# Optimization experiments

Measured on AMD Instinct MI355X. Metric: run time of the kernel, lower is better.

The kernel has to match this reference:

```python
import jax, jax.numpy as jnp
import numpy as np

T_, B_, DIM, NB, D, H_, W_ = 4, 4, 256, 16, 16, 32, 32
VTH_L1_LOW = VTH_L1_HIGH = 0.5
EPS = 1e-5

# ---- surrogate-gradient spike (ATan surrogate, alpha=2.0, spikingjelly default) ----
@jax.custom_vjp
def spike(x):
    return (x >= 0).astype(x.dtype)

def _spk_fwd(x):
    return spike(x), x

def _spk_bwd(x, g):
    a = 2.0
    return (g * (a / 2.0) / (1.0 + (jnp.pi / 2.0 * a * x) ** 2),)

spike.defvjp(_spk_fwd, _spk_bwd)

def lif(x, tau=2.0, vth=1.0):
    # MultiStepLIFNode: v += (x - v)/tau; fire at vth; hard reset (detach_reset)
    def step(v, xt):
        v = v + (xt - v) / tau
        s = spike(v - vth)
        v = v * (1.0 - jax.lax.stop_gradient(s))
        return v, s
    _, s = jax.lax.scan(step, jnp.zeros_like(x[0]), x)
    return s

def haar_mat(n):
    m = np.zeros((n, n), np.float32)
    s = 1.0 / np.sqrt(2.0)
    for i in range(n // 2):
        m[i, 2 * i] = s; m[i, 2 * i + 1] = s          # low-pass rows
        m[n // 2 + i, 2 * i] = s; m[n // 2 + i, 2 * i + 1] = -s  # high-pass rows
    return jnp.asarray(m)

def bn(x, g, b):  # training-mode BatchNorm2d over (N,C,H,W)
    mu = jnp.mean(x, axis=(0, 2, 3), keepdims=True)
    var = jnp.var(x, axis=(0, 2, 3), keepdims=True)
    return g.reshape(1, -1, 1, 1) * (x - mu) * jax.lax.rsqrt(var + EPS) + b.reshape(1, -1, 1, 1)

def conv(x, w, b):
    y = jax.lax.conv_general_dilated(x, w, (1, 1), 'SAME',
                                     dimension_numbers=('NCHW', 'OIHW', 'NCHW'))
    return y + b.reshape(1, -1, 1, 1)

def band_gate(c, vth, tau):
    # coefficient spiking threshold then channel-energy sparsity gate
    c = c * spike(jnp.abs(c) - vth)
    E = jnp.mean(c * c, axis=(-2, -1), keepdims=True)  # per (T,B,C) energy
    return c * (E > tau).astype(c.dtype)

def _forward(x, haar_weight, conv1_w, conv1_b, conv2_w, conv2_b,
             bn_fwd_g, bn_fwd_b, bn_mul_g, bn_mul_b, bn_inv_g, bn_inv_b,
             bn_c1_g, bn_c1_b, bn_c2_g, bn_c2_b):
    T, B, C, H, W = x.shape
    HmW, HmH = haar_mat(W), haar_mat(H)
    Hh, Wh, TB = H // 2, W // 2, T * B
    s = lif(x)
    # ---- level-1 Haar along W ----
    y = jnp.einsum('vw,tbchw->tbchv', HmW, s)
    low, high = y[..., :Wh], y[..., Wh:]
    low = low * spike(jnp.abs(low) - VTH_L1_LOW)
    high = high * spike(jnp.abs(high) - VTH_L1_HIGH)
    l1 = jnp.concatenate([low, high], axis=2)  # (T,B,2C,H,Wh)
    l1 = bn(l1.reshape(TB, 2 * C, H, Wh), bn_fwd_g, bn_fwd_b).reshape(T, B, 2 * C, H, Wh)
    # ---- level-2 Haar along H + per-band sparsity ----
    lo, hi = l1[:, :, :C], l1[:, :, C:]
    zlo = jnp.einsum('vh,tbchw->tbcvw', HmH, lo)
    zhi = jnp.einsum('vh,tbchw->tbcvw', HmH, hi)
    LL = band_gate(zlo[..., :Hh, :], 0.5, 0.01)
    HL = band_gate(zlo[..., Hh:, :], 0.5, 0.02)
    LH = band_gate(zhi[..., :Hh, :], 0.5, 0.02)
    HH = band_gate(zhi[..., Hh:, :], 0.5, 0.05)
    l2 = jnp.concatenate([LL, HL, LH, HH], axis=2)  # (T,B,4C,Hh,Wh)
    l2 = bn(l2.reshape(TB, 4 * C, Hh, Wh), bn_mul_g, bn_mul_b)
    # ---- block-diagonal multiply ----
    h = l2.reshape(TB, NB, 4 * D, Hh, Wh).transpose(0, 3, 4, 1, 2)  # (TB,Hh,Wh,NB,4D)
    parts = [jnp.einsum('thwbd,bdk->thwbk', h[..., i * D:(i + 1) * D], haar_weight)
             for i in range(4)]
    h = jnp.concatenate(parts, axis=-1)
    h = h.reshape(TB, Hh, Wh, 4 * C).transpose(0, 3, 1, 2).reshape(T, B, 4 * C, Hh, Wh)
    # ---- inverse Haar ----
    LLc, HLc, LHc, HHc = h[:, :, :C], h[:, :, C:2 * C], h[:, :, 2 * C:3 * C], h[:, :, 3 * C:]
    lo = jnp.einsum('vh,tbcvw->tbchw', HmH, jnp.concatenate([LLc, HLc], axis=-2))
    hi = jnp.einsum('vh,tbcvw->tbchw', HmH, jnp.concatenate([LHc, HHc], axis=-2))
    rec = jnp.einsum('vw,tbchv->tbchw', HmW, jnp.concatenate([lo, hi], axis=-1))
    rec = bn(rec.reshape(TB, C, H, W), bn_inv_g, bn_inv_b).reshape(T, B, C, H, W)
    # ---- conv residual paths over block channels ----
    xr = s.reshape(TB * NB, D, H, W)
    c1 = bn(conv(xr, conv1_w, conv1_b).reshape(TB, C, H, W), bn_c1_g, bn_c1_b).reshape(T, B, C, H, W)
    c2 = bn(conv(xr, conv2_w, conv2_b).reshape(TB, C, H, W), bn_c2_g, bn_c2_b).reshape(T, B, C, H, W)
    return rec + c1 + c2

def setup_inputs() -> dict:
    key = jax.random.key(0)
    ks = jax.random.split(key, 4)
    return {
        'x': jax.random.normal(ks[0], (T_, B_, DIM, H_, W_), jnp.float32),
        'haar_weight': 0.02 * jax.random.normal(ks[1], (NB, D, D), jnp.float32),
        'conv1_w': 0.1 * jax.random.normal(ks[2], (D, D, 1, 1), jnp.float32),
        'conv1_b': jnp.zeros((D,), jnp.float32),
        'conv2_w': 0.05 * jax.random.normal(ks[3], (D, D, 3, 3), jnp.float32),
        'conv2_b': jnp.zeros((D,), jnp.float32),
        'bn_fwd_g': jnp.ones((2 * DIM,), jnp.float32), 'bn_fwd_b': jnp.zeros((2 * DIM,), jnp.float32),
        'bn_mul_g': jnp.ones((4 * DIM,), jnp.float32), 'bn_mul_b': jnp.zeros((4 * DIM,), jnp.float32),
        'bn_inv_g': jnp.ones((DIM,), jnp.float32), 'bn_inv_b': jnp.zeros((DIM,), jnp.float32),
        'bn_c1_g': jnp.ones((DIM,), jnp.float32), 'bn_c1_b': jnp.zeros((DIM,), jnp.float32),
        'bn_c2_g': jnp.ones((DIM,), jnp.float32), 'bn_c2_b': jnp.zeros((DIM,), jnp.float32),
    }

def reference(x, haar_weight, conv1_w, conv1_b, conv2_w, conv2_b,
              bn_fwd_g, bn_fwd_b, bn_mul_g, bn_mul_b, bn_inv_g, bn_inv_b,
              bn_c1_g, bn_c1_b, bn_c2_g, bn_c2_b):
    return _forward(x, haar_weight, conv1_w, conv1_b, conv2_w, conv2_b,
                    bn_fwd_g, bn_fwd_b, bn_mul_g, bn_mul_b, bn_inv_g, bn_inv_b,
                    bn_c1_g, bn_c1_b, bn_c2_g, bn_c2_b)
```

## Files before the change

### kernel.cpp

```cpp
#include <hip/hip_runtime.h>
#include <hip/hip_bf16.h>

#define T_ 4
#define B_ 4
#define C_ 256
#define H_ 32
#define W_ 32
#define TB_ 16
#define Hh_ 16
#define Wh_ 16
#define INVS2 0.70710678118654752440f
#define EPSBN 1e-5f

#define OFF_HW   0
#define OFF_W1   4096
#define OFF_B1   4352
#define OFF_W2   4368
#define OFF_B2   6672
#define OFF_G1   6688
#define OFF_BE1  7200
#define OFF_G2   7712
#define OFF_BE2  8736
#define OFF_G3   9760
#define OFF_BE3  10016
#define OFF_G4   10272
#define OFF_BE4  10528
#define OFF_G5   10784
#define OFF_BE5  11040
#define W_TOTAL  11296
#define NSUMS    4608

struct WPtrs { const void* p[15]; };

typedef __attribute__((ext_vector_type(8))) short short8;
typedef __attribute__((ext_vector_type(4))) float f32x4;

__device__ inline float bf2f(__hip_bfloat16 v) { return __bfloat162float(v); }
__device__ inline float bfu(unsigned short u) { return __uint_as_float((unsigned)u << 16); }

__global__ __launch_bounds__(256) void k_prep(const unsigned short* __restrict__ xr,
                                              WPtrs wp,
                                              __hip_bfloat16* __restrict__ wc,
                                              float* __restrict__ sums,
                                              int* __restrict__ flag) {
    int tid = threadIdx.x;
    int cnt = 0;
    for (int i = tid; i < 2048; i += 256) {
        int e = (xr[i] >> 7) & 0xFF;
        if (e >= 134) cnt++;
    }
    for (int o = 1; o < 64; o <<= 1) cnt += __shfl_xor(cnt, o, 64);
    __shared__ int sh[4];
    if ((tid & 63) == 0) sh[tid >> 6] = cnt;
    __syncthreads();
    int f = (sh[0] + sh[1] + sh[2] + sh[3] >= 32) ? 1 : 0;
    if (blockIdx.x == 0 && tid == 0) *flag = f;

    const int sizes[15] = {4096, 256, 16, 2304, 16, 512, 512, 1024, 1024,
                           256, 256, 256, 256, 256, 256};
    int i = blockIdx.x * 256 + tid;
    if (i < W_TOTAL) {
        int seg = 0, off = 0;
        while (i >= off + sizes[seg]) { off += sizes[seg]; seg++; }
        int j = i - off;
        float v = f ? ((const float*)wp.p[seg])[j]
                    : bf2f(((const __hip_bfloat16*)wp.p[seg])[j]);
        wc[i] = __float2bfloat16(v);
    }
    if (i < NSUMS) sums[i] = 0.f;
}

__global__ __launch_bounds__(256) void k_lifhaar(const void* __restrict__ x_,
                                                 const int* __restrict__ flag,
                                                 unsigned char* __restrict__ s,
                                                 signed char* __restrict__ l1,
                                                 float* __restrict__ sums1) {
    int bid = blockIdx.x;
    int tid = threadIdx.x;
    int half = bid & 1;
    int c = (bid >> 1) & 255;
    int b = bid >> 9;
    int wp = tid & 15;
    int hl = tid >> 4;
    int h = half * 16 + hl;
    int f = *flag;
    const float* xf = (const float*)x_;
    const unsigned int* xb = (const unsigned int*)x_;
    int n = ((b * 256 + c) * 32 + h) * 32 + 2 * wp;

    float v0 = 0.f, v1 = 0.f;
    float aL = 0.f, qL = 0.f, aH = 0.f, qH = 0.f;
    #pragma unroll
    for (int t = 0; t < T_; ++t) {
        size_t idx = (size_t)t * 1048576 + n;
        float x0, x1;
        if (f) {
            float2 xx = *(const float2*)(xf + idx);
            x0 = xx.x; x1 = xx.y;
        } else {
            unsigned int u = xb[idx >> 1];
            x0 = __uint_as_float(u << 16);
            x1 = __uint_as_float(u & 0xffff0000u);
        }
        v0 += (x0 - v0) * 0.5f;
        v1 += (x1 - v1) * 0.5f;
        float s0 = (v0 >= 1.f) ? 1.f : 0.f;
        float s1 = (v1 >= 1.f) ? 1.f : 0.f;
        v0 *= (1.f - s0);
        v1 *= (1.f - s1);
        int tb = t * 4 + b;
        ((uchar2*)s)[(size_t)(tb * 256 + c) * 512 + h * 16 + wp] =
            make_uchar2((unsigned char)s0, (unsigned char)s1);
        float cl = s0 + s1, ch = s0 - s1;
        size_t lb = (((size_t)tb * 512 + c) * 32 + h) * 16 + wp;
        l1[lb] = (signed char)(int)cl;
        l1[lb + (size_t)256 * 512] = (signed char)(int)ch;
        aL += cl; qL += cl * cl; aH += ch; qH += ch * ch;
    }
    for (int o = 1; o < 64; o <<= 1) {
        aL += __shfl_xor(aL, o, 64); qL += __shfl_xor(qL, o, 64);
        aH += __shfl_xor(aH, o, 64); qH += __shfl_xor(qH, o, 64);
    }
    __shared__ float part[4][4];
    int lane = tid & 63, wv = tid >> 6;
    if (lane == 0) {
        part[wv][0] = aL; part[wv][1] = qL; part[wv][2] = aH; part[wv][3] = qH;
    }
    __syncthreads();
    if (tid < 4) {
        float tot = part[0][tid] + part[1][tid] + part[2][tid] + part[3][tid];
        const int offs[4] = {0, 512, 256, 768};
        atomicAdd(&sums1[offs[tid] + c], tot);
    }
}

struct SharedU {
    union {
        struct {
            short lo[1025 * 8];
            short hi[1025 * 8];
            unsigned short w2s[2304];
            unsigned short w1s[256];
            unsigned short bs[32];
            float parts[4][4][16];
        } cv;
        struct {
            float lo[512];
            float hi[512];
            float part[4][8];
        } s2;
    };
};

__global__ __launch_bounds__(256) void k_work(const unsigned char* __restrict__ s,
                                              const signed char* __restrict__ l1,
                                              const float* __restrict__ sums1,
                                              const __hip_bfloat16* __restrict__ wc,
                                              float* __restrict__ stats,
                                              __hip_bfloat16* __restrict__ l2,
                                              __hip_bfloat16* __restrict__ c1,
                                              __hip_bfloat16* __restrict__ c2) {
    __shared__ SharedU sm;
    int bid = blockIdx.x;
    int tid = threadIdx.x;
    int lane = tid & 63, wv = tid >> 6;

    if (bid < 256) {
        int img = bid;
        const unsigned short* wr = (const unsigned short*)wc;
        for (int i = tid; i < 2304; i += 256) sm.cv.w2s[i] = wr[OFF_W2 + i];
        sm.cv.w1s[tid] = wr[OFF_W1 + tid];
        if (tid < 16) { sm.cv.bs[tid] = wr[OFF_B1 + tid]; sm.cv.bs[16 + tid] = wr[OFF_B2 + tid]; }
        if (tid < 8) {
            ((unsigned int*)sm.cv.lo)[4096 + (tid & 3)] = 0;
            ((unsigned int*)sm.cv.hi)[4096 + (tid & 3)] = 0;
        }
        {
            const unsigned int* sp = (const unsigned int*)(s + (size_t)img * 16384);
            int d2 = tid >> 5;
            int pg = tid & 31;
            unsigned int* dst = (unsigned int*)((d2 < 4) ? sm.cv.lo : sm.cv.hi);
            int dl = d2 & 3;
            #pragma unroll
            for (int p = 0; p < 8; ++p) {
                int base = p * 32 + pg;
                unsigned int u0 = sp[d2 * 512 + base];
                unsigned int u1 = sp[d2 * 512 + 256 + base];
                #pragma unroll
                for (int jj = 0; jj < 4; ++jj) {
                    int j = (jj + pg) & 3;
                    unsigned int b0 = (u0 >> (8 * j)) & 255u;
                    unsigned int b1 = (u1 >> (8 * j)) & 255u;
                    unsigned int val = (b0 ? 0x3F80u : 0u) | ((b1 ? 0x3F80u : 0u) << 16);
                    int pix = p * 128 + pg * 4 + j;
                    dst[pix * 4 + dl] = val;
                }
            }
        }
        __syncthreads();

        int m = lane & 15;
        int g = lane >> 4;
        const int tapA[5] = {0, 2, 4, 6, 8};
        const int tapB[5] = {1, 3, 5, 7, 8};

        short8 afr[5], a1f;
        #pragma unroll
        for (int p = 0; p < 5; ++p) {
            int tap = (g < 2) ? tapA[p] : tapB[p];
            short8 av;
            #pragma unroll
            for (int j = 0; j < 8; ++j) {
                int d = (g & 1) * 8 + j;
                unsigned short w = sm.cv.w2s[m * 144 + d * 9 + tap];
                if (p == 4 && g >= 2) w = 0;
                av[j] = (short)w;
            }
            afr[p] = av;
        }
        #pragma unroll
        for (int j = 0; j < 8; ++j) {
            int d = (g & 1) * 8 + j;
            a1f[j] = (g < 2) ? (short)sm.cv.w1s[m * 16 + d] : (short)0;
        }
        float bias1[4], bias2[4];
        #pragma unroll
        for (int r = 0; r < 4; ++r) {
            bias1[r] = bfu(sm.cv.bs[g * 4 + r]);
            bias2[r] = bfu(sm.cv.bs[16 + g * 4 + r]);
        }

        __hip_bfloat16* o1 = c1 + (size_t)img * 16384;
        __hip_bfloat16* o2 = c2 + (size_t)img * 16384;
        const short* bsrc = (g & 1) ? sm.cv.hi : sm.cv.lo;

        float cs1[4] = {0, 0, 0, 0}, cq1[4] = {0, 0, 0, 0};
        float cs2[4] = {0, 0, 0, 0}, cq2[4] = {0, 0, 0, 0};

        for (int t = wv * 16; t < wv * 16 + 16; ++t) {
            int h = t >> 1;
            int w0 = (t & 1) << 4;
            f32x4 acc2 = {0.f, 0.f, 0.f, 0.f};
            f32x4 acc1 = {0.f, 0.f, 0.f, 0.f};
            #pragma unroll
            for (int p = 0; p < 5; ++p) {
                int tap = (g < 2) ? tapA[p] : tapB[p];
                int row = h + tap / 3 - 1;
                int col = w0 + m + (tap % 3) - 1;
                bool ok = ((unsigned)row < 32u) && ((unsigned)col < 32u);
                int idx = ok ? (row * 32 + col) : 1024;
                short8 bv = *(const short8*)&bsrc[idx * 8];
                acc2 = __builtin_amdgcn_mfma_f32_16x16x32_bf16(afr[p], bv, acc2, 0, 0, 0);
                if (p == 2)
                    acc1 = __builtin_amdgcn_mfma_f32_16x16x32_bf16(a1f, bv, acc1, 0, 0, 0);
            }
            int pix = h * 32 + w0 + m;
            #pragma unroll
            for (int r = 0; r < 4; ++r) {
                int k = g * 4 + r;
                float y1 = acc1[r] + bias1[r];
                float y2 = acc2[r] + bias2[r];
                o1[(size_t)k * 1024 + pix] = __float2bfloat16(y1);
                o2[(size_t)k * 1024 + pix] = __float2bfloat16(y2);
                cs1[r] += y1; cq1[r] += y1 * y1;
                cs2[r] += y2; cq2[r] += y2 * y2;
            }
        }
        #pragma unroll
        for (int o = 1; o < 16; o <<= 1) {
            #pragma unroll
            for (int r = 0; r < 4; ++r) {
                cs1[r] += __shfl_xor(cs1[r], o, 64);
                cq1[r] += __shfl_xor(cq1[r], o, 64);
                cs2[r] += __shfl_xor(cs2[r], o, 64);
                cq2[r] += __shfl_xor(cq2[r], o, 64);
            }
        }
        if (m == 0) {
            #pragma unroll
            for (int r = 0; r < 4; ++r) {
                sm.cv.parts[wv][g][r * 4 + 0] = cs1[r];
                sm.cv.parts[wv][g][r * 4 + 1] = cq1[r];
                sm.cv.parts[wv][g][r * 4 + 2] = cs2[r];
                sm.cv.parts[wv][g][r * 4 + 3] = cq2[r];
            }
        }
        __syncthreads();
        if (tid < 64) {
            int gg = tid >> 4, r = (tid >> 2) & 3, which = tid & 3;
            float tot = sm.cv.parts[0][gg][r * 4 + which] + sm.cv.parts[1][gg][r * 4 + which]
                      + sm.cv.parts[2][gg][r * 4 + which] + sm.cv.parts[3][gg][r * 4 + which];
            int ch = (img & 15) * 16 + gg * 4 + r;
            const int base[4] = {3584, 3840, 4096, 4352};
            atomicAdd(&stats[base[which] + ch], tot);
        }
    } else {
        int blk = bid - 256;
        int c = blk & 255;
        int tb = blk >> 8;

        const float nrm = 1.f / 8192.f;
        float mL = sums1[c] * INVS2 * nrm;
        float vL = fmaxf(sums1[512 + c] * 0.5f * nrm - mL * mL, 0.f);
        float sL = bf2f(wc[OFF_G1 + c]) * rsqrtf(vL + EPSBN);
        float tL = bf2f(wc[OFF_BE1 + c]) - mL * sL;
        float mH = sums1[256 + c] * INVS2 * nrm;
        float vH = fmaxf(sums1[768 + c] * 0.5f * nrm - mH * mH, 0.f);
        float sH = bf2f(wc[OFF_G1 + 256 + c]) * rsqrtf(vH + EPSBN);
        float tH = bf2f(wc[OFF_BE1 + 256 + c]) - mH * sH;

        const signed char* plo = l1 + (((size_t)tb * 512) + c) * (H_ * Wh_);
        const signed char* phi = l1 + (((size_t)tb * 512) + 256 + c) * (H_ * Wh_);
        float slo = sL * INVS2, shi = sH * INVS2;
        sm.s2.lo[tid & 511] = 0.f;
        {
            sm.s2.lo[tid]       = (float)plo[tid] * slo + tL;
            sm.s2.hi[tid]       = (float)phi[tid] * shi + tH;
            sm.s2.lo[tid + 256] = (float)plo[tid + 256] * slo + tL;
            sm.s2.hi[tid + 256] = (float)phi[tid + 256] * shi + tH;
        }
        __syncthreads();

        int w = tid & 15, v = tid >> 4;
        float a = sm.s2.lo[(2 * v) * Wh_ + w], b = sm.s2.lo[(2 * v + 1) * Wh_ + w];
        float zLL = (a + b) * INVS2;
        float zHL = (a - b) * INVS2;
        a = sm.s2.hi[(2 * v) * Wh_ + w]; b = sm.s2.hi[(2 * v + 1) * Wh_ + w];
        float zLH = (a + b) * INVS2;
        float zHH = (a - b) * INVS2;
        zLL = (fabsf(zLL) - 0.5f >= 0.f) ? zLL : 0.f;
        zHL = (fabsf(zHL) - 0.5f >= 0.f) ? zHL : 0.f;
        zLH = (fabsf(zLH) - 0.5f >= 0.f) ? zLH : 0.f;
        zHH = (fabsf(zHH) - 0.5f >= 0.f) ? zHH : 0.f;

        float r0 = zLL, r1 = zHL, r2 = zLH, r3 = zHH;
        float q0 = zLL * zLL, q1 = zHL * zHL, q2 = zLH * zLH, q3 = zHH * zHH;
        for (int o = 1; o < 64; o <<= 1) {
            r0 += __shfl_xor(r0, o, 64); r1 += __shfl_xor(r1, o, 64);
            r2 += __shfl_xor(r2, o, 64); r3 += __shfl_xor(r3, o, 64);
            q0 += __shfl_xor(q0, o, 64); q1 += __shfl_xor(q1, o, 64);
            q2 += __shfl_xor(q2, o, 64); q3 += __shfl_xor(q3, o, 64);
        }
        if (lane == 0) {
            sm.s2.part[wv][0] = r0; sm.s2.part[wv][1] = r1;
            sm.s2.part[wv][2] = r2; sm.s2.part[wv][3] = r3;
            sm.s2.part[wv][4] = q0; sm.s2.part[wv][5] = q1;
            sm.s2.part[wv][6] = q2; sm.s2.part[wv][7] = q3;
        }
        __syncthreads();
        float S0 = sm.s2.part[0][0] + sm.s2.part[1][0] + sm.s2.part[2][0] + sm.s2.part[3][0];
        float S1 = sm.s2.part[0][1] + sm.s2.part[1][1] + sm.s2.part[2][1] + sm.s2.part[3][1];
        float S2 = sm.s2.part[0][2] + sm.s2.part[1][2] + sm.s2.part[2][2] + sm.s2.part[3][2];
        float S3 = sm.s2.part[0][3] + sm.s2.part[1][3] + sm.s2.part[2][3] + sm.s2.part[3][3];
        float Q0 = sm.s2.part[0][4] + sm.s2.part[1][4] + sm.s2.part[2][4] + sm.s2.part[3][4];
        float Q1 = sm.s2.part[0][5] + sm.s2.part[1][5] + sm.s2.part[2][5] + sm.s2.part[3][5];
        float Q2 = sm.s2.part[0][6] + sm.s2.part[1][6] + sm.s2.part[2][6] + sm.s2.part[3][6];
        float Q3 = sm.s2.part[0][7] + sm.s2.part[1][7] + sm.s2.part[2][7] + sm.s2.part[3][7];
        float fLL = (Q0 * (1.f / 256.f) > 0.01f) ? 1.f : 0.f;
        float fHL = (Q1 * (1.f / 256.f) > 0.02f) ? 1.f : 0.f;
        float fLH = (Q2 * (1.f / 256.f) > 0.02f) ? 1.f : 0.f;
        float fHH = (Q3 * (1.f / 256.f) > 0.05f) ? 1.f : 0.f;

        float* sums2 = stats + 1024;
        if (tid < 8) {
            const int cho[8] = {0, 1024, 256, 1280, 512, 1536, 768, 1792};
            const float vals[8] = {fLL * S0, fLL * Q0, fHL * S1, fHL * Q1,
                                   fLH * S2, fLH * Q2, fHH * S3, fHH * Q3};
            atomicAdd(&sums2[cho[tid] + c], vals[tid]);
        }

        size_t ob = (((size_t)tb * 1024) + c) * 256 + tid;
        l2[ob]               = __float2bfloat16(zLL * fLL);
        l2[ob + 256u * 256u] = __float2bfloat16(zHL * fHL);
        l2[ob + 512u * 256u] = __float2bfloat16(zLH * fLH);
        l2[ob + 768u * 256u] = __float2bfloat16(zHH * fHH);
    }
}

__global__ __launch_bounds__(256) void k_mixinv(const __hip_bfloat16* __restrict__ l2,
                                                const __hip_bfloat16* __restrict__ wc,
                                                float* __restrict__ stats,
                                                __hip_bfloat16* __restrict__ rec) {
    int bid = blockIdx.x;
    int cg = bid & 15;
    int tb = bid >> 4;
    int tid = threadIdx.x;
    int lane = tid & 63, wvv = tid >> 6;
    const float* sums2 = stats + 1024;

    __shared__ float wt[4][16][16];
    __shared__ float bsc[64], bsh[64];
    __shared__ float parts2[4][32];
    for (int i = tid; i < 1024; i += 256) {
        int q = i >> 8, rem = i & 255, d = rem >> 4, k = rem & 15;
        int nb = q * 4 + (cg >> 2);
        wt[q][d][k] = bf2f(wc[OFF_HW + nb * 256 + d * 16 + k]);
    }
    if (tid < 64) {
        int q = tid >> 4, d = tid & 15;
        int ch = q * 256 + cg * 16 + d;
        float m = sums2[ch] * (1.f / 4096.f);
        float var = fmaxf(sums2[1024 + ch] * (1.f / 4096.f) - m * m, 0.f);
        float sc = bf2f(wc[OFF_G2 + ch]) * rsqrtf(var + EPSBN);
        bsc[tid] = sc;
        bsh[tid] = bf2f(wc[OFF_BE2 + ch]) - m * sc;
    }
    __syncthreads();

    float h[4][16];
    #pragma unroll
    for (int q = 0; q < 4; ++q)
        #pragma unroll
        for (int k = 0; k < 16; ++k) h[q][k] = 0.f;

    int p = tid;
    #pragma unroll
    for (int q = 0; q < 4; ++q) {
        const __hip_bfloat16* base =
            l2 + ((size_t)tb * 1024 + q * 256 + cg * 16) * 256 + p;
        #pragma unroll
        for (int d = 0; d < 16; ++d) {
            float xv = bf2f(base[d * 256]) * bsc[q * 16 + d] + bsh[q * 16 + d];
            #pragma unroll
            for (int k = 0; k < 16; ++k)
                h[q][k] = fmaf(xv, wt[q][d][k], h[q][k]);
        }
    }

    int uh = tid >> 4, uw = tid & 15;
    __hip_bfloat16* ob = rec + ((size_t)tb * 256 + cg * 16) * 1024;
    float sk[16], qk[16];
    #pragma unroll
    for (int k = 0; k < 16; ++k) {
        float LL = h[0][k], HL = h[1][k], LH = h[2][k], HH = h[3][k];
        float v00 = 0.5f * (LL + HL + LH + HH);
        float v01 = 0.5f * (LL + HL - LH - HH);
        float v10 = 0.5f * (LL - HL + LH - HH);
        float v11 = 0.5f * (LL - HL - LH + HH);
        __hip_bfloat162 top, bot;
        top.x = __float2bfloat16(v00); top.y = __float2bfloat16(v01);
        bot.x = __float2bfloat16(v10); bot.y = __float2bfloat16(v11);
        *(__hip_bfloat162*)(ob + (size_t)k * 1024 + (2 * uh) * 32 + 2 * uw) = top;
        *(__hip_bfloat162*)(ob + (size_t)k * 1024 + (2 * uh + 1) * 32 + 2 * uw) = bot;
        sk[k] = v00 + v01 + v10 + v11;
        qk[k] = v00 * v00 + v01 * v01 + v10 * v10 + v11 * v11;
    }
    for (int o = 1; o < 64; o <<= 1) {
        #pragma unroll
        for (int k = 0; k < 16; ++k) {
            sk[k] += __shfl_xor(sk[k], o, 64);
            qk[k] += __shfl_xor(qk[k], o, 64);
        }
    }
    if (lane == 0) {
        #pragma unroll
        for (int k = 0; k < 16; ++k) {
            parts2[wvv][k * 2]     = sk[k];
            parts2[wvv][k * 2 + 1] = qk[k];
        }
    }
    __syncthreads();
    if (tid < 32) {
        int k = tid >> 1, which = tid & 1;
        float tot = parts2[0][tid] + parts2[1][tid] + parts2[2][tid] + parts2[3][tid];
        atomicAdd(&stats[3072 + which * 256 + cg * 16 + k], tot);
    }
}

__global__ __launch_bounds__(256) void k_final(const __hip_bfloat16* __restrict__ rec,
                                               const __hip_bfloat16* __restrict__ c1,
                                               const __hip_bfloat16* __restrict__ c2,
                                               const float* __restrict__ stats,
                                               const __hip_bfloat16* __restrict__ wc,
                                               const int* __restrict__ flag,
                                               void* __restrict__ out_) {
    int n2 = blockIdx.x * 256 + threadIdx.x;
    int c = ((n2 * 2) >> 10) & 255;
    const float inv = 1.f / 16384.f;
    float m3 = stats[3072 + c] * inv;
    float v3 = fmaxf(stats[3328 + c] * inv - m3 * m3, 0.f);
    float sc3 = bf2f(wc[OFF_G3 + c]) * rsqrtf(v3 + EPSBN);
    float sh3 = bf2f(wc[OFF_BE3 + c]) - m3 * sc3;
    float m4 = stats[3584 + c] * inv;
    float v4 = fmaxf(stats[3840 + c] * inv - m4 * m4, 0.f);
    float sc4 = bf2f(wc[OFF_G4 + c]) * rsqrtf(v4 + EPSBN);
    float sh4 = bf2f(wc[OFF_BE4 + c]) - m4 * sc4;
    float m5 = stats[4096 + c] * inv;
    float v5 = fmaxf(stats[4352 + c] * inv - m5 * m5, 0.f);
    float sc5 = bf2f(wc[OFF_G5 + c]) * rsqrtf(v5 + EPSBN);
    float sh5 = bf2f(wc[OFF_BE5 + c]) - m5 * sc5;

    __hip_bfloat162 r = ((const __hip_bfloat162*)rec)[n2];
    __hip_bfloat162 a = ((const __hip_bfloat162*)c1)[n2];
    __hip_bfloat162 b = ((const __hip_bfloat162*)c2)[n2];
    float v0 = bf2f(r.x) * sc3 + sh3 + bf2f(a.x) * sc4 + sh4 + bf2f(b.x) * sc5 + sh5;
    float v1 = bf2f(r.y) * sc3 + sh3 + bf2f(a.y) * sc4 + sh4 + bf2f(b.y) * sc5 + sh5;
    if (*flag) {
        ((float2*)out_)[n2] = make_float2(v0, v1);
    } else {
        __hip_bfloat162 o;
        o.x = __float2bfloat16(v0); o.y = __float2bfloat16(v1);
        ((__hip_bfloat162*)out_)[n2] = o;
    }
}

extern "C" void kernel_launch(void* const* d_in, const int* in_sizes, int n_in,
                              void* d_out, int out_size, void* d_ws, size_t ws_size,
                              hipStream_t stream) {
    char* ws = (char*)d_ws;
    unsigned char* s_u8  = (unsigned char*)ws;
    signed char* l1c     = (signed char*)(ws + ((size_t)4 << 20));
    __hip_bfloat16* l2   = (__hip_bfloat16*)(ws + ((size_t)8 << 20));
    __hip_bfloat16* rec  = (__hip_bfloat16*)(ws + ((size_t)16 << 20));
    __hip_bfloat16* c1   = (__hip_bfloat16*)(ws + ((size_t)24 << 20));
    __hip_bfloat16* c2   = (__hip_bfloat16*)(ws + ((size_t)32 << 20));
    __hip_bfloat16* wc   = (__hip_bfloat16*)(ws + ((size_t)40 << 20));
    float* stats         = (float*)(ws + ((size_t)40 << 20) + (64 << 10));
    int* flag            = (int*)(ws + ((size_t)40 << 20) + (128 << 10));

    WPtrs wp;
    for (int i = 0; i < 15; ++i) wp.p[i] = d_in[i + 1];

    dim3 blk(256);
    k_prep<<<dim3(45), blk, 0, stream>>>((const unsigned short*)d_in[0], wp, wc, stats, flag);
    k_lifhaar<<<dim3(2048), blk, 0, stream>>>(d_in[0], flag, s_u8, l1c, stats);
    k_work<<<dim3(4352), blk, 0, stream>>>(s_u8, l1c, stats, wc, stats, l2, c1, c2);
    k_mixinv<<<dim3(256), blk, 0, stream>>>(l2, wc, stats, rec);
    k_final<<<dim3(8192), blk, 0, stream>>>(rec, c1, c2, stats, wc, flag, d_out);
}
```

Baseline: 149.7 us.

## Recompute conv branches in final kernel instead of storing intermediates

The conv1/conv2 outputs are no longer written to global memory in the work kernel, which now keeps only their BN statistics. A new final kernel, one block per image, recomputes both convolutions with MFMA from the spike tensor and fuses the BN affine transforms and the three-way sum into the output write. This removes two 8 MB bf16 intermediate writes and their reads, at the cost of running the conv MFMAs twice. The final kernel now has only 256 blocks, so it has less parallelism than the 8192-block elementwise kernel it replaces.

```diff
diff --git a/kernel.cpp b/kernel.cpp
--- a/kernel.cpp
+++ b/kernel.cpp
@@ -157,9 +157,7 @@
                                               const float* __restrict__ sums1,
                                               const __hip_bfloat16* __restrict__ wc,
                                               float* __restrict__ stats,
-                                              __hip_bfloat16* __restrict__ l2,
-                                              __hip_bfloat16* __restrict__ c1,
-                                              __hip_bfloat16* __restrict__ c2) {
+                                              __hip_bfloat16* __restrict__ l2) {
     __shared__ SharedU sm;
     int bid = blockIdx.x;
     int tid = threadIdx.x;
@@ -230,8 +228,6 @@
             bias2[r] = bfu(sm.cv.bs[16 + g * 4 + r]);
         }
 
-        __hip_bfloat16* o1 = c1 + (size_t)img * 16384;
-        __hip_bfloat16* o2 = c2 + (size_t)img * 16384;
         const short* bsrc = (g & 1) ? sm.cv.hi : sm.cv.lo;
 
         float cs1[4] = {0, 0, 0, 0}, cq1[4] = {0, 0, 0, 0};
@@ -254,14 +250,10 @@
                 if (p == 2)
                     acc1 = __builtin_amdgcn_mfma_f32_16x16x32_bf16(a1f, bv, acc1, 0, 0, 0);
             }
-            int pix = h * 32 + w0 + m;
             #pragma unroll
             for (int r = 0; r < 4; ++r) {
-                int k = g * 4 + r;
                 float y1 = acc1[r] + bias1[r];
                 float y2 = acc2[r] + bias2[r];
-                o1[(size_t)k * 1024 + pix] = __float2bfloat16(y1);
-                o2[(size_t)k * 1024 + pix] = __float2bfloat16(y2);
                 cs1[r] += y1; cq1[r] += y1 * y1;
                 cs2[r] += y2; cq2[r] += y2 * y2;
             }
@@ -467,40 +459,151 @@
     }
 }
 
-__global__ __launch_bounds__(256) void k_final(const __hip_bfloat16* __restrict__ rec,
-                                               const __hip_bfloat16* __restrict__ c1,
-                                               const __hip_bfloat16* __restrict__ c2,
-                                               const float* __restrict__ stats,
-                                               const __hip_bfloat16* __restrict__ wc,
-                                               const int* __restrict__ flag,
-                                               void* __restrict__ out_) {
-    int n2 = blockIdx.x * 256 + threadIdx.x;
-    int c = ((n2 * 2) >> 10) & 255;
-    const float inv = 1.f / 16384.f;
-    float m3 = stats[3072 + c] * inv;
-    float v3 = fmaxf(stats[3328 + c] * inv - m3 * m3, 0.f);
-    float sc3 = bf2f(wc[OFF_G3 + c]) * rsqrtf(v3 + EPSBN);
-    float sh3 = bf2f(wc[OFF_BE3 + c]) - m3 * sc3;
-    float m4 = stats[3584 + c] * inv;
-    float v4 = fmaxf(stats[3840 + c] * inv - m4 * m4, 0.f);
-    float sc4 = bf2f(wc[OFF_G4 + c]) * rsqrtf(v4 + EPSBN);
-    float sh4 = bf2f(wc[OFF_BE4 + c]) - m4 * sc4;
-    float m5 = stats[4096 + c] * inv;
-    float v5 = fmaxf(stats[4352 + c] * inv - m5 * m5, 0.f);
-    float sc5 = bf2f(wc[OFF_G5 + c]) * rsqrtf(v5 + EPSBN);
-    float sh5 = bf2f(wc[OFF_BE5 + c]) - m5 * sc5;
-
-    __hip_bfloat162 r = ((const __hip_bfloat162*)rec)[n2];
-    __hip_bfloat162 a = ((const __hip_bfloat162*)c1)[n2];
-    __hip_bfloat162 b = ((const __hip_bfloat162*)c2)[n2];
-    float v0 = bf2f(r.x) * sc3 + sh3 + bf2f(a.x) * sc4 + sh4 + bf2f(b.x) * sc5 + sh5;
-    float v1 = bf2f(r.y) * sc3 + sh3 + bf2f(a.y) * sc4 + sh4 + bf2f(b.y) * sc5 + sh5;
-    if (*flag) {
-        ((float2*)out_)[n2] = make_float2(v0, v1);
-    } else {
-        __hip_bfloat162 o;
-        o.x = __float2bfloat16(v0); o.y = __float2bfloat16(v1);
-        ((__hip_bfloat162*)out_)[n2] = o;
+struct FinSh {
+    short lo[1025 * 8];
+    short hi[1025 * 8];
+    unsigned short w2s[2304];
+    unsigned short w1s[256];
+    unsigned short bs[32];
+    float sc3[16], sc4[16], sc5[16], shS[16];
+};
+
+__global__ __launch_bounds__(256) void k_final2(const unsigned char* __restrict__ s,
+                                                const __hip_bfloat16* __restrict__ rec,
+                                                const float* __restrict__ stats,
+                                                const __hip_bfloat16* __restrict__ wc,
+                                                const int* __restrict__ flag,
+                                                void* __restrict__ out_) {
+    __shared__ FinSh sm;
+    int img = blockIdx.x;
+    int tid = threadIdx.x;
+    int lane = tid & 63, wv = tid >> 6;
+
+    const unsigned short* wr = (const unsigned short*)wc;
+    for (int i = tid; i < 2304; i += 256) sm.w2s[i] = wr[OFF_W2 + i];
+    sm.w1s[tid] = wr[OFF_W1 + tid];
+    if (tid < 16) { sm.bs[tid] = wr[OFF_B1 + tid]; sm.bs[16 + tid] = wr[OFF_B2 + tid]; }
+    if (tid < 8) {
+        ((unsigned int*)sm.lo)[4096 + (tid & 3)] = 0;
+        ((unsigned int*)sm.hi)[4096 + (tid & 3)] = 0;
+    }
+    if (tid >= 32 && tid < 48) {
+        int k = tid - 32;
+        int c = (img & 15) * 16 + k;
+        const float inv = 1.f / 16384.f;
+        float m3 = stats[3072 + c] * inv;
+        float v3 = fmaxf(stats[3328 + c] * inv - m3 * m3, 0.f);
+        float sc3 = bf2f(wc[OFF_G3 + c]) * rsqrtf(v3 + EPSBN);
+        float sh3 = bf2f(wc[OFF_BE3 + c]) - m3 * sc3;
+        float m4 = stats[3584 + c] * inv;
+        float v4 = fmaxf(stats[3840 + c] * inv - m4 * m4, 0.f);
+        float sc4 = bf2f(wc[OFF_G4 + c]) * rsqrtf(v4 + EPSBN);
+        float sh4 = bf2f(wc[OFF_BE4 + c]) - m4 * sc4;
+        float m5 = stats[4096 + c] * inv;
+        float v5 = fmaxf(stats[4352 + c] * inv - m5 * m5, 0.f);
+        float sc5 = bf2f(wc[OFF_G5 + c]) * rsqrtf(v5 + EPSBN);
+        float sh5 = bf2f(wc[OFF_BE5 + c]) - m5 * sc5;
+        sm.sc3[k] = sc3;
+        sm.sc4[k] = sc4;
+        sm.sc5[k] = sc5;
+        sm.shS[k] = sh3 + sh4 + sh5;
+    }
+    {
+        const unsigned int* sp = (const unsigned int*)(s + (size_t)img * 16384);
+        int d2 = tid >> 5;
+        int pg = tid & 31;
+        unsigned int* dst = (unsigned int*)((d2 < 4) ? sm.lo : sm.hi);
+        int dl = d2 & 3;
+        #pragma unroll
+        for (int p = 0; p < 8; ++p) {
+            int base = p * 32 + pg;
+            unsigned int u0 = sp[d2 * 512 + base];
+            unsigned int u1 = sp[d2 * 512 + 256 + base];
+            #pragma unroll
+            for (int jj = 0; jj < 4; ++jj) {
+                int j = (jj + pg) & 3;
+                unsigned int b0 = (u0 >> (8 * j)) & 255u;
+                unsigned int b1 = (u1 >> (8 * j)) & 255u;
+                unsigned int val = (b0 ? 0x3F80u : 0u) | ((b1 ? 0x3F80u : 0u) << 16);
+                int pix = p * 128 + pg * 4 + j;
+                dst[pix * 4 + dl] = val;
+            }
+        }
+    }
+    __syncthreads();
+
+    int m = lane & 15;
+    int g = lane >> 4;
+    const int tapA[5] = {0, 2, 4, 6, 8};
+    const int tapB[5] = {1, 3, 5, 7, 8};
+
+    short8 afr[5], a1f;
+    #pragma unroll
+    for (int p = 0; p < 5; ++p) {
+        int tap = (g < 2) ? tapA[p] : tapB[p];
+        short8 av;
+        #pragma unroll
+        for (int j = 0; j < 8; ++j) {
+            int d = (g & 1) * 8 + j;
+            unsigned short w = sm.w2s[m * 144 + d * 9 + tap];
+            if (p == 4 && g >= 2) w = 0;
+            av[j] = (short)w;
+        }
+        afr[p] = av;
+    }
+    #pragma unroll
+    for (int j = 0; j < 8; ++j) {
+        int d = (g & 1) * 8 + j;
+        a1f[j] = (g < 2) ? (short)sm.w1s[m * 16 + d] : (short)0;
+    }
+    float bias1[4], bias2[4], c3[4], c4[4], c5[4], cS[4];
+    #pragma unroll
+    for (int r = 0; r < 4; ++r) {
+        int k = g * 4 + r;
+        bias1[r] = bfu(sm.bs[k]);
+        bias2[r] = bfu(sm.bs[16 + k]);
+        c3[r] = sm.sc3[k];
+        c4[r] = sm.sc4[k];
+        c5[r] = sm.sc5[k];
+        cS[r] = sm.shS[k];
+    }
+
+    const short* bsrc = (g & 1) ? sm.hi : sm.lo;
+    const __hip_bfloat16* rb = rec + (size_t)img * 16384;
+    int f = *flag;
+    float* of = (float*)out_;
+    __hip_bfloat16* ob = (__hip_bfloat16*)out_;
+    size_t obase = (size_t)img * 16384;
+
+    for (int t = wv * 16; t < wv * 16 + 16; ++t) {
+        int hh = t >> 1;
+        int w0 = (t & 1) << 4;
+        f32x4 acc2 = {0.f, 0.f, 0.f, 0.f};
+        f32x4 acc1 = {0.f, 0.f, 0.f, 0.f};
+        #pragma unroll
+        for (int p = 0; p < 5; ++p) {
+            int tap = (g < 2) ? tapA[p] : tapB[p];
+            int row = hh + tap / 3 - 1;
+            int col = w0 + m + (tap % 3) - 1;
+            bool ok = ((unsigned)row < 32u) && ((unsigned)col < 32u);
+            int idx = ok ? (row * 32 + col) : 1024;
+            short8 bv = *(const short8*)&bsrc[idx * 8];
+            acc2 = __builtin_amdgcn_mfma_f32_16x16x32_bf16(afr[p], bv, acc2, 0, 0, 0);
+            if (p == 2)
+                acc1 = __builtin_amdgcn_mfma_f32_16x16x32_bf16(a1f, bv, acc1, 0, 0, 0);
+        }
+        int pix = hh * 32 + w0 + m;
+        #pragma unroll
+        for (int r = 0; r < 4; ++r) {
+            int k = g * 4 + r;
+            float y1 = acc1[r] + bias1[r];
+            float y2 = acc2[r] + bias2[r];
+            float rv = bf2f(rb[(size_t)k * 1024 + pix]);
+            float o = rv * c3[r] + y1 * c4[r] + y2 * c5[r] + cS[r];
+            size_t oi = obase + (size_t)k * 1024 + pix;
+            if (f) of[oi] = o;
+            else   ob[oi] = __float2bfloat16(o);
+        }
     }
 }
 
@@ -512,8 +615,6 @@
     signed char* l1c     = (signed char*)(ws + ((size_t)4 << 20));
     __hip_bfloat16* l2   = (__hip_bfloat16*)(ws + ((size_t)8 << 20));
     __hip_bfloat16* rec  = (__hip_bfloat16*)(ws + ((size_t)16 << 20));
-    __hip_bfloat16* c1   = (__hip_bfloat16*)(ws + ((size_t)24 << 20));
-    __hip_bfloat16* c2   = (__hip_bfloat16*)(ws + ((size_t)32 << 20));
     __hip_bfloat16* wc   = (__hip_bfloat16*)(ws + ((size_t)40 << 20));
     float* stats         = (float*)(ws + ((size_t)40 << 20) + (64 << 10));
     int* flag            = (int*)(ws + ((size_t)40 << 20) + (128 << 10));
@@ -524,7 +625,7 @@
     dim3 blk(256);
     k_prep<<<dim3(45), blk, 0, stream>>>((const unsigned short*)d_in[0], wp, wc, stats, flag);
     k_lifhaar<<<dim3(2048), blk, 0, stream>>>(d_in[0], flag, s_u8, l1c, stats);
-    k_work<<<dim3(4352), blk, 0, stream>>>(s_u8, l1c, stats, wc, stats, l2, c1, c2);
+    k_work<<<dim3(4352), blk, 0, stream>>>(s_u8, l1c, stats, wc, stats, l2);
     k_mixinv<<<dim3(256), blk, 0, stream>>>(l2, wc, stats, rec);
-    k_final<<<dim3(8192), blk, 0, stream>>>(rec, c1, c2, stats, wc, flag, d_out);
+    k_final2<<<dim3(256), blk, 0, stream>>>(s_u8, rec, stats, wc, flag, d_out);
 }
```

Result: slower. 159.6 us (+6.6%).

## Fuse prep into LIF-Haar kernel, replace atomics with partials, split mixinv over k

Applied to the files above, without the earlier changes.

Merges the weight-conversion/zeroing prep kernel into the LIF+Haar kernel as extra blocks, with each block recomputing the dtype flag locally so one launch and its dependency are removed. Level-1 band statistics are now written as per-block partial slots rather than accumulated with atomics, and k_work sums the 8 slots itself. k_mixinv is split four ways along the output-channel dimension (1024 blocks instead of 256), which cuts registers per thread and raises parallelism but repeats the input loads four times.

```diff
diff --git a/kernel.cpp b/kernel.cpp
--- a/kernel.cpp
+++ b/kernel.cpp
@@ -29,6 +29,7 @@
 #define OFF_BE5  11040
 #define W_TOTAL  11296
 #define NSUMS    4608
+#define P1OFF    4608
 
 struct WPtrs { const void* p[15]; };
 
@@ -38,12 +39,17 @@
 __device__ inline float bf2f(__hip_bfloat16 v) { return __bfloat162float(v); }
 __device__ inline float bfu(unsigned short u) { return __uint_as_float((unsigned)u << 16); }
 
-__global__ __launch_bounds__(256) void k_prep(const unsigned short* __restrict__ xr,
-                                              WPtrs wp,
-                                              __hip_bfloat16* __restrict__ wc,
-                                              float* __restrict__ sums,
-                                              int* __restrict__ flag) {
+__global__ __launch_bounds__(256) void k_lifprep(const void* __restrict__ x_,
+                                                 WPtrs wp,
+                                                 __hip_bfloat16* __restrict__ wc,
+                                                 float* __restrict__ stats,
+                                                 int* __restrict__ flag,
+                                                 unsigned char* __restrict__ s,
+                                                 signed char* __restrict__ l1) {
+    int bid = blockIdx.x;
     int tid = threadIdx.x;
+
+    const unsigned short* xr = (const unsigned short*)x_;
     int cnt = 0;
     for (int i = tid; i < 2048; i += 256) {
         int e = (xr[i] >> 7) & 0xFF;
@@ -51,42 +57,38 @@
     }
     for (int o = 1; o < 64; o <<= 1) cnt += __shfl_xor(cnt, o, 64);
     __shared__ int sh[4];
+    __shared__ float part[4][4];
     if ((tid & 63) == 0) sh[tid >> 6] = cnt;
     __syncthreads();
     int f = (sh[0] + sh[1] + sh[2] + sh[3] >= 32) ? 1 : 0;
-    if (blockIdx.x == 0 && tid == 0) *flag = f;
-
-    const int sizes[15] = {4096, 256, 16, 2304, 16, 512, 512, 1024, 1024,
-                           256, 256, 256, 256, 256, 256};
-    int i = blockIdx.x * 256 + tid;
-    if (i < W_TOTAL) {
-        int seg = 0, off = 0;
-        while (i >= off + sizes[seg]) { off += sizes[seg]; seg++; }
-        int j = i - off;
-        float v = f ? ((const float*)wp.p[seg])[j]
-                    : bf2f(((const __hip_bfloat16*)wp.p[seg])[j]);
-        wc[i] = __float2bfloat16(v);
-    }
-    if (i < NSUMS) sums[i] = 0.f;
-}
-
-__global__ __launch_bounds__(256) void k_lifhaar(const void* __restrict__ x_,
-                                                 const int* __restrict__ flag,
-                                                 unsigned char* __restrict__ s,
-                                                 signed char* __restrict__ l1,
-                                                 float* __restrict__ sums1) {
-    int bid = blockIdx.x;
-    int tid = threadIdx.x;
+
+    if (bid >= 2048) {
+        int pb = bid - 2048;
+        if (pb == 0 && tid == 0) *flag = f;
+        const int sizes[15] = {4096, 256, 16, 2304, 16, 512, 512, 1024, 1024,
+                               256, 256, 256, 256, 256, 256};
+        int i = pb * 256 + tid;
+        if (i < W_TOTAL) {
+            int seg = 0, off = 0;
+            while (i >= off + sizes[seg]) { off += sizes[seg]; seg++; }
+            int j = i - off;
+            float v = f ? ((const float*)wp.p[seg])[j]
+                        : bf2f(((const __hip_bfloat16*)wp.p[seg])[j]);
+            wc[i] = __float2bfloat16(v);
+        }
+        if (i < 3584) stats[1024 + i] = 0.f;
+        return;
+    }
+
     int half = bid & 1;
     int c = (bid >> 1) & 255;
     int b = bid >> 9;
-    int wp = tid & 15;
+    int wp_ = tid & 15;
     int hl = tid >> 4;
     int h = half * 16 + hl;
-    int f = *flag;
     const float* xf = (const float*)x_;
     const unsigned int* xb = (const unsigned int*)x_;
-    int n = ((b * 256 + c) * 32 + h) * 32 + 2 * wp;
+    int n = ((b * 256 + c) * 32 + h) * 32 + 2 * wp_;
 
     float v0 = 0.f, v1 = 0.f;
     float aL = 0.f, qL = 0.f, aH = 0.f, qH = 0.f;
@@ -109,10 +111,10 @@
         v0 *= (1.f - s0);
         v1 *= (1.f - s1);
         int tb = t * 4 + b;
-        ((uchar2*)s)[(size_t)(tb * 256 + c) * 512 + h * 16 + wp] =
+        ((uchar2*)s)[(size_t)(tb * 256 + c) * 512 + h * 16 + wp_] =
             make_uchar2((unsigned char)s0, (unsigned char)s1);
         float cl = s0 + s1, ch = s0 - s1;
-        size_t lb = (((size_t)tb * 512 + c) * 32 + h) * 16 + wp;
+        size_t lb = (((size_t)tb * 512 + c) * 32 + h) * 16 + wp_;
         l1[lb] = (signed char)(int)cl;
         l1[lb + (size_t)256 * 512] = (signed char)(int)ch;
         aL += cl; qL += cl * cl; aH += ch; qH += ch * ch;
@@ -121,7 +123,6 @@
         aL += __shfl_xor(aL, o, 64); qL += __shfl_xor(qL, o, 64);
         aH += __shfl_xor(aH, o, 64); qH += __shfl_xor(qH, o, 64);
     }
-    __shared__ float part[4][4];
     int lane = tid & 63, wv = tid >> 6;
     if (lane == 0) {
         part[wv][0] = aL; part[wv][1] = qL; part[wv][2] = aH; part[wv][3] = qH;
@@ -129,8 +130,7 @@
     __syncthreads();
     if (tid < 4) {
         float tot = part[0][tid] + part[1][tid] + part[2][tid] + part[3][tid];
-        const int offs[4] = {0, 512, 256, 768};
-        atomicAdd(&sums1[offs[tid] + c], tot);
+        stats[P1OFF + ((b * 2 + half) * 4 + tid) * 256 + c] = tot;
     }
 }
 
@@ -154,7 +154,6 @@
 
 __global__ __launch_bounds__(256) void k_work(const unsigned char* __restrict__ s,
                                               const signed char* __restrict__ l1,
-                                              const float* __restrict__ sums1,
                                               const __hip_bfloat16* __restrict__ wc,
                                               float* __restrict__ stats,
                                               __hip_bfloat16* __restrict__ l2,
@@ -299,13 +298,23 @@
         int c = blk & 255;
         int tb = blk >> 8;
 
+        const float* p1 = stats + P1OFF;
+        float aLs = 0.f, qLs = 0.f, aHs = 0.f, qHs = 0.f;
+        #pragma unroll
+        for (int slot = 0; slot < 8; ++slot) {
+            aLs += p1[(slot * 4 + 0) * 256 + c];
+            qLs += p1[(slot * 4 + 1) * 256 + c];
+            aHs += p1[(slot * 4 + 2) * 256 + c];
+            qHs += p1[(slot * 4 + 3) * 256 + c];
+        }
+
         const float nrm = 1.f / 8192.f;
-        float mL = sums1[c] * INVS2 * nrm;
-        float vL = fmaxf(sums1[512 + c] * 0.5f * nrm - mL * mL, 0.f);
+        float mL = aLs * INVS2 * nrm;
+        float vL = fmaxf(qLs * 0.5f * nrm - mL * mL, 0.f);
         float sL = bf2f(wc[OFF_G1 + c]) * rsqrtf(vL + EPSBN);
         float tL = bf2f(wc[OFF_BE1 + c]) - mL * sL;
-        float mH = sums1[256 + c] * INVS2 * nrm;
-        float vH = fmaxf(sums1[768 + c] * 0.5f * nrm - mH * mH, 0.f);
+        float mH = aHs * INVS2 * nrm;
+        float vH = fmaxf(qHs * 0.5f * nrm - mH * mH, 0.f);
         float sH = bf2f(wc[OFF_G1 + 256 + c]) * rsqrtf(vH + EPSBN);
         float tH = bf2f(wc[OFF_BE1 + 256 + c]) - mH * sH;
 
@@ -382,19 +391,22 @@
                                                 float* __restrict__ stats,
                                                 __hip_bfloat16* __restrict__ rec) {
     int bid = blockIdx.x;
-    int cg = bid & 15;
-    int tb = bid >> 4;
+    int ks = bid & 3;
+    int cg = (bid >> 2) & 15;
+    int tb = bid >> 6;
     int tid = threadIdx.x;
     int lane = tid & 63, wvv = tid >> 6;
     const float* sums2 = stats + 1024;
 
-    __shared__ float wt[4][16][16];
+    __shared__ float wt[4][16][4];
     __shared__ float bsc[64], bsh[64];
-    __shared__ float parts2[4][32];
-    for (int i = tid; i < 1024; i += 256) {
-        int q = i >> 8, rem = i & 255, d = rem >> 4, k = rem & 15;
+    __shared__ float parts2[4][8];
+    {
+        int i = tid;
+        int q = i >> 6, rem = i & 63, d = rem >> 2, kk = rem & 3;
         int nb = q * 4 + (cg >> 2);
-        wt[q][d][k] = bf2f(wc[OFF_HW + nb * 256 + d * 16 + k]);
+        int k = ks * 4 + kk;
+        wt[q][d][kk] = bf2f(wc[OFF_HW + nb * 256 + d * 16 + k]);
     }
     if (tid < 64) {
         int q = tid >> 4, d = tid & 15;
@@ -407,11 +419,11 @@
     }
     __syncthreads();
 
-    float h[4][16];
+    float h[4][4];
     #pragma unroll
     for (int q = 0; q < 4; ++q)
         #pragma unroll
-        for (int k = 0; k < 16; ++k) h[q][k] = 0.f;
+        for (int kk = 0; kk < 4; ++kk) h[q][kk] = 0.f;
 
     int p = tid;
     #pragma unroll
@@ -422,17 +434,18 @@
         for (int d = 0; d < 16; ++d) {
             float xv = bf2f(base[d * 256]) * bsc[q * 16 + d] + bsh[q * 16 + d];
             #pragma unroll
-            for (int k = 0; k < 16; ++k)
-                h[q][k] = fmaf(xv, wt[q][d][k], h[q][k]);
+            for (int kk = 0; kk < 4; ++kk)
+                h[q][kk] = fmaf(xv, wt[q][d][kk], h[q][kk]);
         }
     }
 
     int uh = tid >> 4, uw = tid & 15;
     __hip_bfloat16* ob = rec + ((size_t)tb * 256 + cg * 16) * 1024;
-    float sk[16], qk[16];
+    float sk[4], qk[4];
     #pragma unroll
-    for (int k = 0; k < 16; ++k) {
-        float LL = h[0][k], HL = h[1][k], LH = h[2][k], HH = h[3][k];
+    for (int kk = 0; kk < 4; ++kk) {
+        int k = ks * 4 + kk;
+        float LL = h[0][kk], HL = h[1][kk], LH = h[2][kk], HH = h[3][kk];
         float v00 = 0.5f * (LL + HL + LH + HH);
         float v01 = 0.5f * (LL + HL - LH - HH);
         float v10 = 0.5f * (LL - HL + LH - HH);
@@ -442,28 +455,28 @@
         bot.x = __float2bfloat16(v10); bot.y = __float2bfloat16(v11);
         *(__hip_bfloat162*)(ob + (size_t)k * 1024 + (2 * uh) * 32 + 2 * uw) = top;
         *(__hip_bfloat162*)(ob + (size_t)k * 1024 + (2 * uh + 1) * 32 + 2 * uw) = bot;
-        sk[k] = v00 + v01 + v10 + v11;
-        qk[k] = v00 * v00 + v01 * v01 + v10 * v10 + v11 * v11;
+        sk[kk] = v00 + v01 + v10 + v11;
+        qk[kk] = v00 * v00 + v01 * v01 + v10 * v10 + v11 * v11;
     }
     for (int o = 1; o < 64; o <<= 1) {
         #pragma unroll
-        for (int k = 0; k < 16; ++k) {
-            sk[k] += __shfl_xor(sk[k], o, 64);
-            qk[k] += __shfl_xor(qk[k], o, 64);
+        for (int kk = 0; kk < 4; ++kk) {
+            sk[kk] += __shfl_xor(sk[kk], o, 64);
+            qk[kk] += __shfl_xor(qk[kk], o, 64);
         }
     }
     if (lane == 0) {
         #pragma unroll
-        for (int k = 0; k < 16; ++k) {
-            parts2[wvv][k * 2]     = sk[k];
-            parts2[wvv][k * 2 + 1] = qk[k];
+        for (int kk = 0; kk < 4; ++kk) {
+            parts2[wvv][kk * 2]     = sk[kk];
+            parts2[wvv][kk * 2 + 1] = qk[kk];
         }
     }
     __syncthreads();
-    if (tid < 32) {
-        int k = tid >> 1, which = tid & 1;
+    if (tid < 8) {
+        int kk = tid >> 1, which = tid & 1;
         float tot = parts2[0][tid] + parts2[1][tid] + parts2[2][tid] + parts2[3][tid];
-        atomicAdd(&stats[3072 + which * 256 + cg * 16 + k], tot);
+        atomicAdd(&stats[3072 + which * 256 + cg * 16 + ks * 4 + kk], tot);
     }
 }
 
@@ -522,9 +535,8 @@
     for (int i = 0; i < 15; ++i) wp.p[i] = d_in[i + 1];
 
     dim3 blk(256);
-    k_prep<<<dim3(45), blk, 0, stream>>>((const unsigned short*)d_in[0], wp, wc, stats, flag);
-    k_lifhaar<<<dim3(2048), blk, 0, stream>>>(d_in[0], flag, s_u8, l1c, stats);
-    k_work<<<dim3(4352), blk, 0, stream>>>(s_u8, l1c, stats, wc, stats, l2, c1, c2);
-    k_mixinv<<<dim3(256), blk, 0, stream>>>(l2, wc, stats, rec);
+    k_lifprep<<<dim3(2093), blk, 0, stream>>>(d_in[0], wp, wc, stats, flag, s_u8, l1c);
+    k_work<<<dim3(4352), blk, 0, stream>>>(s_u8, l1c, wc, stats, l2, c1, c2);
+    k_mixinv<<<dim3(1024), blk, 0, stream>>>(l2, wc, stats, rec);
     k_final<<<dim3(8192), blk, 0, stream>>>(rec, c1, c2, stats, wc, flag, d_out);
 }
```

Result: faster. 145.8 us (-2.6%).
